# Performance work log

Measured on AMD Instinct MI355X. Metric: run time of the kernel, lower is better.

Reference implementation:

```python
import jax, jax.numpy as jnp
import numpy as np

_LOG2PI = float(np.log(2.0 * np.pi))


def setup_inputs() -> dict:
    key = jax.random.key(0)
    ks = jax.random.split(key, 9)
    B, T, S, A, O = 64, 128, 512, 16, 4096
    regime = jax.random.randint(ks[0], (B,), 0, 2).astype(jnp.float32)
    obs = jax.random.randint(ks[1], (T + 1, B), 0, O, dtype=jnp.int32)
    rewards = jax.random.normal(ks[2], (T + 1, B), jnp.float32)
    dones = jnp.zeros((T + 1, B), jnp.float32)
    actions = jax.random.randint(ks[3], (T, B), 0, A, dtype=jnp.int32)
    prior_logits = jax.random.normal(ks[4], (S,), jnp.float32)
    trans_logits = jax.random.normal(ks[5], (A, S, S), jnp.float32)
    obs_logits = jax.random.normal(ks[6], (S, O), jnp.float32)
    policy_logits = jax.random.normal(ks[7], (S, A), jnp.float32)
    r_mu = jax.random.normal(ks[8], (S,), jnp.float32)
    r_logsig = jnp.zeros((S,), jnp.float32)
    return {"regime": regime, "obs": obs, "rewards": rewards, "dones": dones,
            "actions": actions, "prior_logits": prior_logits,
            "trans_logits": trans_logits, "obs_logits": obs_logits,
            "policy_logits": policy_logits, "r_mu": r_mu, "r_logsig": r_logsig}


def _log_prob(regime, obs, rewards, dones, actions, prior_logits, trans_logits,
              obs_logits, policy_logits, r_mu, r_logsig):
    # normalized log-prob tables (tabular instantiation of AugmentedModel)
    log_prior = jax.nn.log_softmax(prior_logits)              # [S]
    log_trans = jax.nn.log_softmax(trans_logits, axis=-1)     # [A,S,S]
    log_obs = jax.nn.log_softmax(obs_logits, axis=-1)         # [S,O]
    log_pol = jax.nn.log_softmax(policy_logits, axis=-1)      # [S,A]
    lse = jax.scipy.special.logsumexp

    def emis(o, r):  # log q(o|s) + log q(r|s) -> [B,S]
        lo = log_obs.T[o]                                      # [B,S] gather
        lr = (-0.5 * (((r[:, None] - r_mu[None, :]) * jnp.exp(-r_logsig)[None, :]) ** 2)
              - r_logsig[None, :] - 0.5 * _LOG2PI)             # [B,S]
        return lo + lr

    def act_term(a, done):  # masked log q(a|s) -> [B,S]
        la = log_pol.T[a]                                      # [B,S]
        la = jnp.where((done == 1.0)[:, None], jnp.zeros_like(la), la)
        la = jnp.where((regime == 1.0)[:, None], jnp.zeros_like(la), la)
        return la

    T = actions.shape[0]
    B = regime.shape[0]

    # t = 0
    was_done = jnp.zeros((B,), rewards.dtype)
    done0 = dones[0]
    lq_sorda = log_prior[None, :] + emis(obs[0], rewards[0]) + act_term(actions[0], done0)
    lq_orda = lse(lq_sorda, axis=-1) * (1.0 - was_done)        # [B]
    log_prob = lq_orda
    lq_s_h = lq_sorda - lq_orda[:, None]
    # belief propagation through transition: [B,S,1] + [B,S,S] -> lse over prev state
    lq_snext_h = lse(lq_s_h[:, :, None] + log_trans[actions[0]], axis=1)

    def step(carry, xs):  # t = 1 .. T-1 (has an action)
        log_prob, was_done, lq_s_hprev = carry
        o, r, d, a = xs
        done = jnp.maximum(was_done, d)
        lq = lq_s_hprev + emis(o, r) + act_term(a, done)
        lq_orda = lse(lq, axis=-1) * (1.0 - was_done)
        log_prob = jnp.where(jnp.isinf(log_prob), log_prob, log_prob + lq_orda)
        lq_s_h = lq - lq_orda[:, None]
        lq_snext = lse(lq_s_h[:, :, None] + log_trans[a], axis=1)
        return (log_prob, done, lq_snext), None

    xs = (obs[1:T], rewards[1:T], dones[1:T], actions[1:T])
    (log_prob, was_done, lq_s_hprev), _ = jax.lax.scan(
        step, (log_prob, done0, lq_snext_h), xs)

    # final step t = T (no action term)
    lq = lq_s_hprev + emis(obs[T], rewards[T])
    lq_ord = lse(lq, axis=-1) * (1.0 - was_done)
    log_prob = jnp.where(jnp.isinf(log_prob), log_prob, log_prob + lq_ord)
    return log_prob


def reference(regime, obs, rewards, dones, actions, prior_logits, trans_logits,
              obs_logits, policy_logits, r_mu, r_logsig):
    return _log_prob(regime, obs, rewards, dones, actions, prior_logits,
                     trans_logits, obs_logits, policy_logits, r_mu, r_logsig)
```

## Files before the change

### kernel.cpp

```cpp
#include <hip/hip_runtime.h>
#include <math.h>

#define DI __device__ __forceinline__

constexpr int BB = 64;
constexpr int TT = 128;
constexpr int SS = 512;
constexpr int AA = 16;
constexpr int OO = 4096;
constexpr float LOG2PI = 1.8378770664093453f;
constexpr float LOG4096 = 8.317766166719343f;

typedef float f32x4 __attribute__((ext_vector_type(4)));

DI void lds_barrier() {
    asm volatile("s_waitcnt lgkmcnt(0)\n\ts_barrier" ::: "memory");
}

DI unsigned int f32_to_e4m3(float x) {
    unsigned int u = __float_as_uint(x);
    unsigned int lsb = (u >> 20) & 1u;
    unsigned int rounded = u + 0x7ffffu + lsb;
    int e8 = (int)(rounded >> 23) - 120;
    unsigned int m3 = (rounded >> 20) & 7u;
    unsigned int norm = ((unsigned int)e8 << 3) | m3;
    int sub = __float2int_rn(x * 512.0f);
    return (e8 <= 0) ? (unsigned int)sub : norm;
}

DI float bflyMax(float v) {
#pragma unroll
    for (int off = 32; off; off >>= 1) v = fmaxf(v, __shfl_xor(v, off));
    return v;
}
DI float bflySum(float v) {
#pragma unroll
    for (int off = 32; off; off >>= 1) v += __shfl_xor(v, off);
    return v;
}
DI float halfMax(float v) {
#pragma unroll
    for (int off = 16; off; off >>= 1) v = fmaxf(v, __shfl_xor(v, off));
    return v;
}
DI float halfSum(float v) {
#pragma unroll
    for (int off = 16; off; off >>= 1) v += __shfl_xor(v, off);
    return v;
}

template <int NW>
DI float blockMax(float v, float* wr) {
    v = bflyMax(v);
    const int lane = threadIdx.x & 63, wv = threadIdx.x >> 6;
    if (lane == 0) wr[wv] = v;
    __syncthreads();
    float r = wr[0];
#pragma unroll
    for (int i = 1; i < NW; ++i) r = fmaxf(r, wr[i]);
    __syncthreads();
    return r;
}
template <int NW>
DI float blockSum(float v, float* wr) {
    v = bflySum(v);
    const int lane = threadIdx.x & 63, wv = threadIdx.x >> 6;
    if (lane == 0) wr[wv] = v;
    __syncthreads();
    float r = wr[0];
#pragma unroll
    for (int i = 1; i < NW; ++i) r += wr[i];
    __syncthreads();
    return r;
}


__global__ __launch_bounds__(1024) void k_pack(const float* __restrict__ tl,
                                               unsigned char* __restrict__ PB) {
    __shared__ unsigned char lds[16384];
    const int a = blockIdx.x >> 4;
    const int kt = blockIdx.x & 15;
    const int tid = threadIdx.x;
    const int r = tid >> 5;
    const int nt = tid & 31;
    const int k = kt * 32 + r;
    const float* row = tl + ((size_t)a * SS + k) * SS + nt * 16;

    float x[16];
#pragma unroll
    for (int i = 0; i < 4; ++i) {
        float4 v = ((const float4*)row)[i];
        x[4 * i] = v.x; x[4 * i + 1] = v.y; x[4 * i + 2] = v.z; x[4 * i + 3] = v.w;
    }
    float mx = -INFINITY;
#pragma unroll
    for (int i = 0; i < 16; ++i) mx = fmaxf(mx, x[i]);
    mx = halfMax(mx);
    float e[16];
    float sm = 0.f;
#pragma unroll
    for (int i = 0; i < 16; ++i) { e[i] = __expf(x[i] - mx); sm += e[i]; }
    sm = halfSum(sm);
    const float scale = 256.0f / sm;

    const int base = (nt >> 1) * 1024 + ((r >> 3) * 16) * 16 + (nt & 1) * 8 + (r & 7);
#pragma unroll
    for (int i = 0; i < 16; ++i) {
        lds[base + i * 16] = (unsigned char)f32_to_e4m3(e[i] * scale);
    }
    __syncthreads();

    ulonglong2* dst = (ulonglong2*)(PB + (size_t)(a * 16 + kt) * 16384);
    dst[tid] = ((const ulonglong2*)lds)[tid];
}

__global__ __launch_bounds__(256) void k_obs_stats(const float* __restrict__ ol,
                                                   float* __restrict__ mo,
                                                   float* __restrict__ lo) {
    __shared__ float wr[4];
    const int s = blockIdx.x;
    const float* in = ol + (size_t)s * OO;
    const int tid = threadIdx.x;
    float mx = -INFINITY;
    for (int i = tid; i < OO; i += 256) mx = fmaxf(mx, in[i]);
    float m = blockMax<4>(mx, wr);
    float sm = 0.f;
    for (int i = tid; i < OO; i += 256) sm += __expf(in[i] - m);
    float sum = blockSum<4>(sm, wr);
    if (tid == 0) { mo[s] = m; lo[s] = __logf(sum); }
}

__global__ __launch_bounds__(256) void k_obsT(const float* __restrict__ ol,
                                              const float* __restrict__ mo,
                                              const float* __restrict__ lo,
                                              float* __restrict__ obsT) {
    __shared__ float tile[64][65];
    const int tO = blockIdx.x % (OO / 64);
    const int tS = blockIdx.x / (OO / 64);
    const int o0 = tO * 64, s0 = tS * 64;
    const int cc = threadIdx.x & 63, rr = threadIdx.x >> 6;
#pragma unroll
    for (int j = 0; j < 16; ++j) {
        int r = rr + j * 4;
        tile[r][cc] = ol[(size_t)(s0 + r) * OO + o0 + cc] - mo[s0 + r] - lo[s0 + r];
    }
    __syncthreads();
#pragma unroll
    for (int j = 0; j < 16; ++j) {
        int r = rr + j * 4;
        obsT[(size_t)(o0 + r) * SS + s0 + cc] = tile[cc][r];
    }
}

__global__ __launch_bounds__(512, 2) void k_main(
    const float* __restrict__ regime, const int* __restrict__ obs,
    const float* __restrict__ rewards, const float* __restrict__ dones,
    const int* __restrict__ actions, const float* __restrict__ prior_logits,
    const unsigned char* __restrict__ PB, const float* __restrict__ obsT,
    const float* __restrict__ policy_logits, const float* __restrict__ r_mu,
    const float* __restrict__ r_logsig, float* __restrict__ out) {
    __shared__ float wrm[8], wrs[8];
    __shared__ unsigned char p8[4 * 144 + 16];
    __shared__ float lqprev[SS];
    __shared__ float polT_l[AA * SS];
    __shared__ int obs_l[TT + 1];
    __shared__ float rew_l[TT + 1];
    __shared__ float done_l[TT + 1];
    __shared__ int act_l[TT];

    const int b = blockIdx.x;
    const int tid = threadIdx.x;
    const int wv = tid >> 6, lane = tid & 63, quad = lane >> 4;
    const int s = tid;

    if (tid <= TT) {
        obs_l[tid] = obs[tid * BB + b];
        rew_l[tid] = rewards[tid * BB + b];
        done_l[tid] = dones[tid * BB + b];
        if (tid < TT) act_l[tid] = actions[tid * BB + b];
    }
    {
        const float4* pr4 = (const float4*)(policy_logits + (size_t)s * AA);
        float4 v0 = pr4[0], v1 = pr4[1], v2 = pr4[2], v3 = pr4[3];
        float xv[16] = {v0.x, v0.y, v0.z, v0.w, v1.x, v1.y, v1.z, v1.w,
                        v2.x, v2.y, v2.z, v2.w, v3.x, v3.y, v3.z, v3.w};
        float mx = xv[0];
#pragma unroll
        for (int i = 1; i < 16; ++i) mx = fmaxf(mx, xv[i]);
        float sm = 0.f;
#pragma unroll
        for (int i = 0; i < 16; ++i) sm += __expf(xv[i] - mx);
        float ls = mx + __logf(sm);
#pragma unroll
        for (int a = 0; a < AA; ++a) polT_l[a * SS + s] = xv[a] - ls;
    }
    const float rm = r_mu[s];
    const float rls = r_logsig[s];
    const float inv_sig = __expf(-rls);
    const float reg = regime[b];

    float px = prior_logits[s];
    {
        float wm0 = bflyMax(px);
        if (lane == 0) wrm[wv] = wm0;
    }
    lds_barrier();
    float pm = wrm[0];
#pragma unroll
    for (int i = 1; i < 8; ++i) pm = fmaxf(pm, wrm[i]);
    {
        float ws0 = bflySum(__expf(px - pm));
        if (lane == 0) wrs[wv] = ws0;
    }
    lds_barrier();
    float psum = wrs[0];
#pragma unroll
    for (int i = 1; i < 8; ++i) psum += wrs[i];
    const float prior_reg = px - pm - __logf(psum);

    float obsv = obsT[(size_t)obs_l[0] * SS + s];

    float log_prob = 0.f;
    float was_done = 0.f;

    for (int t = 0; t < TT; ++t) {
        const float r = rew_l[t];
        const int a = act_l[t];
        const float d = done_l[t];
        const float done = fmaxf(was_done, d);

        const ulonglong2* PBa =
            (const ulonglong2*)(PB + (size_t)a * (SS * SS)) + 2 * wv * 64 + lane;
        ulonglong2 bfA[16], bfB[16];
#pragma unroll
        for (int kt = 0; kt < 16; ++kt) {
            bfA[kt] = PBa[kt * 16 * 64];
            bfB[kt] = PBa[kt * 16 * 64 + 64];
        }
        float obsv_next = obsT[(size_t)obs_l[t + 1] * SS + s];
        __builtin_amdgcn_sched_barrier(0);

        float diff = (r - rm) * inv_sig;
        float emis = obsv - 0.5f * diff * diff - rls - 0.5f * LOG2PI;
        float base_in = (t == 0) ? prior_reg : lqprev[s];
        float la = polT_l[a * SS + s];
        if (done == 1.0f || reg == 1.0f) la = 0.f;
        float lq = base_in + emis + la;

        float wmax = bflyMax(lq);
        if (lane == 0) wrm[wv] = wmax;
        lds_barrier();

        float m = wrm[0];
#pragma unroll
        for (int i = 1; i < 8; ++i) m = fmaxf(m, wrm[i]);

        float ex = __expf(lq - m);
        p8[((s >> 3) & 3) * 144 + (s >> 5) * 8 + (s & 7)] =
            (unsigned char)f32_to_e4m3(ex * 16.0f);
        float wsum = bflySum(ex);
        if (lane == 0) wrs[wv] = wsum;
        lds_barrier();

        float sum = wrs[0];
#pragma unroll
        for (int i = 1; i < 8; ++i) sum += wrs[i];
        float lse = m + __logf(sum);
        float lq_orda = lse * (1.0f - was_done);
        if (!isinf(log_prob)) log_prob += lq_orda;
        was_done = done;

        const float basev = m - lq_orda - LOG4096;
        f32x4 acc0 = {0.f, 0.f, 0.f, 0.f};
        f32x4 acc1 = {0.f, 0.f, 0.f, 0.f};
        f32x4 acc2 = {0.f, 0.f, 0.f, 0.f};
        f32x4 acc3 = {0.f, 0.f, 0.f, 0.f};
#pragma unroll
        for (int kt = 0; kt < 16; ++kt) {
            long af = *(const long long*)(p8 + quad * 144 + kt * 8);
            acc0 = __builtin_amdgcn_mfma_f32_16x16x32_fp8_fp8((long)bfA[kt].x, af, acc0, 0, 0, 0);
            acc1 = __builtin_amdgcn_mfma_f32_16x16x32_fp8_fp8((long)bfA[kt].y, af, acc1, 0, 0, 0);
            acc2 = __builtin_amdgcn_mfma_f32_16x16x32_fp8_fp8((long)bfB[kt].x, af, acc2, 0, 0, 0);
            acc3 = __builtin_amdgcn_mfma_f32_16x16x32_fp8_fp8((long)bfB[kt].y, af, acc3, 0, 0, 0);
        }
        if (lane < 16) {
            lqprev[wv * 64 + lane]      = basev + __logf(acc0[0]);
            lqprev[wv * 64 + 16 + lane] = basev + __logf(acc1[0]);
            lqprev[wv * 64 + 32 + lane] = basev + __logf(acc2[0]);
            lqprev[wv * 64 + 48 + lane] = basev + __logf(acc3[0]);
        }
        lds_barrier();
        obsv = obsv_next;
    }

    {
        const float r = rew_l[TT];
        float diff = (r - rm) * inv_sig;
        float emis = obsv - 0.5f * diff * diff - rls - 0.5f * LOG2PI;
        float lq = lqprev[s] + emis;
        float wmax = bflyMax(lq);
        if (lane == 0) wrm[wv] = wmax;
        lds_barrier();
        float m = wrm[0];
#pragma unroll
        for (int i = 1; i < 8; ++i) m = fmaxf(m, wrm[i]);
        float wsum = bflySum(__expf(lq - m));
        if (lane == 0) wrs[wv] = wsum;
        lds_barrier();
        float sum = wrs[0];
#pragma unroll
        for (int i = 1; i < 8; ++i) sum += wrs[i];
        float lse = m + __logf(sum);
        float lq_ord = lse * (1.0f - was_done);
        if (!isinf(log_prob)) log_prob += lq_ord;
    }

    if (tid == 0) out[b] = log_prob;
}

extern "C" void kernel_launch(void* const* d_in, const int* in_sizes, int n_in,
                              void* d_out, int out_size, void* d_ws, size_t ws_size,
                              hipStream_t stream) {
    const float* regime = (const float*)d_in[0];
    const int* obs = (const int*)d_in[1];
    const float* rewards = (const float*)d_in[2];
    const float* dones = (const float*)d_in[3];
    const int* actions = (const int*)d_in[4];
    const float* prior_logits = (const float*)d_in[5];
    const float* trans_logits = (const float*)d_in[6];
    const float* obs_logits = (const float*)d_in[7];
    const float* policy_logits = (const float*)d_in[8];
    const float* r_mu = (const float*)d_in[9];
    const float* r_logsig = (const float*)d_in[10];
    float* out = (float*)d_out;

    char* ws = (char*)d_ws;
    unsigned char* PB = (unsigned char*)ws;
    float* obsT = (float*)(ws + (size_t)AA * SS * SS);
    float* mo = (float*)(ws + (size_t)AA * SS * SS + (size_t)OO * SS * 4);
    float* lo = mo + SS;

    k_pack<<<256, 1024, 0, stream>>>(trans_logits, PB);
    k_obs_stats<<<SS, 256, 0, stream>>>(obs_logits, mo, lo);
    k_obsT<<<(OO / 64) * (SS / 64), 256, 0, stream>>>(obs_logits, mo, lo, obsT);
    k_main<<<BB, 512, 0, stream>>>(regime, obs, rewards, dones, actions, prior_logits,
                                   PB, obsT, policy_logits, r_mu, r_logsig, out);
}
```

Measured before the change: 568.6 us.

## Split each batch row across four cooperating blocks with global-memory step barrier

Each batch element is now handled by four workgroups, and each one computes a quarter of the next-state columns of the per-step transition matmul. Partial results go to a double-buffered global exchange array, and an atomic counter acts as a per-batch barrier before every step. The trans matrix is repacked so each wave reads a contiguous 128 KB slice per action. This cuts per-block MFMA and load work by four and uses 256 blocks instead of 64. In exchange it adds a global atomic spin-wait every timestep, and it relies on all four blocks being co-resident, which risks deadlock if they are not.

```diff
diff --git a/kernel.cpp b/kernel.cpp
--- a/kernel.cpp
+++ b/kernel.cpp
@@ -110,8 +110,15 @@
     }
     __syncthreads();
 
-    ulonglong2* dst = (ulonglong2*)(PB + (size_t)(a * 16 + kt) * 16384);
-    dst[tid] = ((const ulonglong2*)lds)[tid];
+#pragma unroll
+    for (int c = 0; c < 2; ++c) {
+        int idx = tid + c * 1024;
+        int n = idx >> 6, lane = idx & 63;
+        unsigned long long v =
+            *(const unsigned long long*)(lds + (n >> 1) * 1024 + lane * 16 + (n & 1) * 8);
+        *(unsigned long long*)(PB + (size_t)a * 262144 + n * 8192 +
+                               (kt >> 1) * 1024 + lane * 16 + (kt & 1) * 8) = v;
+    }
 }
 
 __global__ __launch_bounds__(256) void k_obs_stats(const float* __restrict__ ol,
@@ -152,26 +159,31 @@
     }
 }
 
+__global__ void k_init(unsigned int* cnt) { cnt[threadIdx.x] = 0u; }
+
 __global__ __launch_bounds__(512, 2) void k_main(
     const float* __restrict__ regime, const int* __restrict__ obs,
     const float* __restrict__ rewards, const float* __restrict__ dones,
     const int* __restrict__ actions, const float* __restrict__ prior_logits,
     const unsigned char* __restrict__ PB, const float* __restrict__ obsT,
     const float* __restrict__ policy_logits, const float* __restrict__ r_mu,
-    const float* __restrict__ r_logsig, float* __restrict__ out) {
+    const float* __restrict__ r_logsig, float* ex, unsigned int* cnt,
+    float* __restrict__ out) {
     __shared__ float wrm[8], wrs[8];
     __shared__ unsigned char p8[4 * 144 + 16];
-    __shared__ float lqprev[SS];
     __shared__ float polT_l[AA * SS];
     __shared__ int obs_l[TT + 1];
     __shared__ float rew_l[TT + 1];
     __shared__ float done_l[TT + 1];
     __shared__ int act_l[TT];
 
-    const int b = blockIdx.x;
+    const int gb = blockIdx.x;
+    const int b = gb >> 2;
+    const int j = gb & 3;
     const int tid = threadIdx.x;
     const int wv = tid >> 6, lane = tid & 63, quad = lane >> 4;
     const int s = tid;
+    const int n = j * 8 + wv;
 
     if (tid <= TT) {
         obs_l[tid] = obs[tid * BB + b];
@@ -220,29 +232,27 @@
 
     float obsv = obsT[(size_t)obs_l[0] * SS + s];
 
+    float lq_reg = 0.f;
     float log_prob = 0.f;
     float was_done = 0.f;
 
     for (int t = 0; t < TT; ++t) {
         const float r = rew_l[t];
-        const int a = act_l[t];
+        const int a = __builtin_amdgcn_readfirstlane(act_l[t]);
         const float d = done_l[t];
         const float done = fmaxf(was_done, d);
 
-        const ulonglong2* PBa =
-            (const ulonglong2*)(PB + (size_t)a * (SS * SS)) + 2 * wv * 64 + lane;
-        ulonglong2 bfA[16], bfB[16];
-#pragma unroll
-        for (int kt = 0; kt < 16; ++kt) {
-            bfA[kt] = PBa[kt * 16 * 64];
-            bfB[kt] = PBa[kt * 16 * 64 + 64];
-        }
+        const unsigned char* base = PB + (size_t)a * 262144 + n * 8192 + lane * 16;
+        ulonglong2 bf[8];
+#pragma unroll
+        for (int ktp = 0; ktp < 8; ++ktp)
+            bf[ktp] = *(const ulonglong2*)(base + ktp * 1024);
         float obsv_next = obsT[(size_t)obs_l[t + 1] * SS + s];
         __builtin_amdgcn_sched_barrier(0);
 
         float diff = (r - rm) * inv_sig;
         float emis = obsv - 0.5f * diff * diff - rls - 0.5f * LOG2PI;
-        float base_in = (t == 0) ? prior_reg : lqprev[s];
+        float base_in = (t == 0) ? prior_reg : lq_reg;
         float la = polT_l[a * SS + s];
         if (done == 1.0f || reg == 1.0f) la = 0.f;
         float lq = base_in + emis + la;
@@ -250,18 +260,16 @@
         float wmax = bflyMax(lq);
         if (lane == 0) wrm[wv] = wmax;
         lds_barrier();
-
         float m = wrm[0];
 #pragma unroll
         for (int i = 1; i < 8; ++i) m = fmaxf(m, wrm[i]);
 
-        float ex = __expf(lq - m);
+        float exv = __expf(lq - m);
         p8[((s >> 3) & 3) * 144 + (s >> 5) * 8 + (s & 7)] =
-            (unsigned char)f32_to_e4m3(ex * 16.0f);
-        float wsum = bflySum(ex);
+            (unsigned char)f32_to_e4m3(exv * 16.0f);
+        float wsum = bflySum(exv);
         if (lane == 0) wrs[wv] = wsum;
         lds_barrier();
-
         float sum = wrs[0];
 #pragma unroll
         for (int i = 1; i < 8; ++i) sum += wrs[i];
@@ -271,25 +279,31 @@
         was_done = done;
 
         const float basev = m - lq_orda - LOG4096;
-        f32x4 acc0 = {0.f, 0.f, 0.f, 0.f};
-        f32x4 acc1 = {0.f, 0.f, 0.f, 0.f};
-        f32x4 acc2 = {0.f, 0.f, 0.f, 0.f};
-        f32x4 acc3 = {0.f, 0.f, 0.f, 0.f};
+        f32x4 acc = {0.f, 0.f, 0.f, 0.f};
 #pragma unroll
         for (int kt = 0; kt < 16; ++kt) {
             long af = *(const long long*)(p8 + quad * 144 + kt * 8);
-            acc0 = __builtin_amdgcn_mfma_f32_16x16x32_fp8_fp8((long)bfA[kt].x, af, acc0, 0, 0, 0);
-            acc1 = __builtin_amdgcn_mfma_f32_16x16x32_fp8_fp8((long)bfA[kt].y, af, acc1, 0, 0, 0);
-            acc2 = __builtin_amdgcn_mfma_f32_16x16x32_fp8_fp8((long)bfB[kt].x, af, acc2, 0, 0, 0);
-            acc3 = __builtin_amdgcn_mfma_f32_16x16x32_fp8_fp8((long)bfB[kt].y, af, acc3, 0, 0, 0);
+            long bh = (kt & 1) ? (long)bf[kt >> 1].y : (long)bf[kt >> 1].x;
+            acc = __builtin_amdgcn_mfma_f32_16x16x32_fp8_fp8(bh, af, acc, 0, 0, 0);
         }
+        float* exb = ex + ((size_t)(t & 1) * BB + b) * SS;
         if (lane < 16) {
-            lqprev[wv * 64 + lane]      = basev + __logf(acc0[0]);
-            lqprev[wv * 64 + 16 + lane] = basev + __logf(acc1[0]);
-            lqprev[wv * 64 + 32 + lane] = basev + __logf(acc2[0]);
-            lqprev[wv * 64 + 48 + lane] = basev + __logf(acc3[0]);
+            __hip_atomic_store(&exb[n * 16 + lane], basev + __logf(acc[0]),
+                               __ATOMIC_RELAXED, __HIP_MEMORY_SCOPE_AGENT);
         }
-        lds_barrier();
+        __syncthreads();
+
+        if (tid == 0) {
+            __hip_atomic_fetch_add(&cnt[b], 1u, __ATOMIC_RELEASE,
+                                   __HIP_MEMORY_SCOPE_AGENT);
+            const unsigned target = 4u * (unsigned)(t + 1);
+            while (__hip_atomic_load(&cnt[b], __ATOMIC_ACQUIRE,
+                                     __HIP_MEMORY_SCOPE_AGENT) < target)
+                __builtin_amdgcn_s_sleep(1);
+        }
+        lds_barrier();
+        lq_reg = __hip_atomic_load(&exb[s], __ATOMIC_RELAXED,
+                                   __HIP_MEMORY_SCOPE_AGENT);
         obsv = obsv_next;
     }
 
@@ -297,7 +311,7 @@
         const float r = rew_l[TT];
         float diff = (r - rm) * inv_sig;
         float emis = obsv - 0.5f * diff * diff - rls - 0.5f * LOG2PI;
-        float lq = lqprev[s] + emis;
+        float lq = lq_reg + emis;
         float wmax = bflyMax(lq);
         if (lane == 0) wrm[wv] = wmax;
         lds_barrier();
@@ -315,7 +329,7 @@
         if (!isinf(log_prob)) log_prob += lq_ord;
     }
 
-    if (tid == 0) out[b] = log_prob;
+    if (j == 0 && tid == 0) out[b] = log_prob;
 }
 
 extern "C" void kernel_launch(void* const* d_in, const int* in_sizes, int n_in,
@@ -339,10 +353,14 @@
     float* obsT = (float*)(ws + (size_t)AA * SS * SS);
     float* mo = (float*)(ws + (size_t)AA * SS * SS + (size_t)OO * SS * 4);
     float* lo = mo + SS;
-
+    unsigned int* cnt = (unsigned int*)(lo + SS);
+    float* ex = (float*)(cnt + 64);
+
+    k_init<<<1, 64, 0, stream>>>(cnt);
     k_pack<<<256, 1024, 0, stream>>>(trans_logits, PB);
     k_obs_stats<<<SS, 256, 0, stream>>>(obs_logits, mo, lo);
     k_obsT<<<(OO / 64) * (SS / 64), 256, 0, stream>>>(obs_logits, mo, lo, obsT);
-    k_main<<<BB, 512, 0, stream>>>(regime, obs, rewards, dones, actions, prior_logits,
-                                   PB, obsT, policy_logits, r_mu, r_logsig, out);
-}
+    k_main<<<BB * 4, 512, 0, stream>>>(regime, obs, rewards, dones, actions,
+                                       prior_logits, PB, obsT, policy_logits,
+                                       r_mu, r_logsig, ex, cnt, out);
+}
```

After: 1.652 ms. 191% more time.

## Stream transition tiles through LDS with async global_load_lds triple buffering

Applied to the files above, without the earlier changes.

Replaces the per-step register prefetch of all sixteen fp8 transition B-fragments with a three-deep ring of direct global-to-LDS loads (global_load_lds) per wave, issuing the next chunk as each chunk's MFMAs run. The policy log-softmax table moves out of shared memory into sixteen registers per thread, with the action picked by a select chain, and launch bounds drop the two-blocks-per-CU hint. The aim is to cut register pressure from the 32 ulonglong2 prefetch buffers and overlap the transition fetch with the MFMA chain. In exchange it uses 48KB more LDS and adds hand-placed vmcnt and lgkmcnt waits, and the vmcnt counts look fragile given the extra obsT load issued after the first DMAs.

```diff
diff --git a/kernel.cpp b/kernel.cpp
--- a/kernel.cpp
+++ b/kernel.cpp
@@ -15,6 +15,12 @@
 
 DI void lds_barrier() {
     asm volatile("s_waitcnt lgkmcnt(0)\n\ts_barrier" ::: "memory");
+}
+
+typedef __attribute__((address_space(3))) unsigned int as3_u32;
+typedef __attribute__((address_space(1))) const unsigned int as1_u32;
+DI void dma1k(const unsigned char* g, unsigned char* l) {
+    __builtin_amdgcn_global_load_lds((as1_u32*)g, (as3_u32*)l, 16, 0, 0);
 }
 
 DI unsigned int f32_to_e4m3(float x) {
@@ -152,17 +158,17 @@
     }
 }
 
-__global__ __launch_bounds__(512, 2) void k_main(
+__global__ __launch_bounds__(512) void k_main(
     const float* __restrict__ regime, const int* __restrict__ obs,
     const float* __restrict__ rewards, const float* __restrict__ dones,
     const int* __restrict__ actions, const float* __restrict__ prior_logits,
     const unsigned char* __restrict__ PB, const float* __restrict__ obsT,
     const float* __restrict__ policy_logits, const float* __restrict__ r_mu,
     const float* __restrict__ r_logsig, float* __restrict__ out) {
+    __shared__ unsigned char stage[3 * 16384];
     __shared__ float wrm[8], wrs[8];
     __shared__ unsigned char p8[4 * 144 + 16];
     __shared__ float lqprev[SS];
-    __shared__ float polT_l[AA * SS];
     __shared__ int obs_l[TT + 1];
     __shared__ float rew_l[TT + 1];
     __shared__ float done_l[TT + 1];
@@ -179,20 +185,23 @@
         done_l[tid] = dones[tid * BB + b];
         if (tid < TT) act_l[tid] = actions[tid * BB + b];
     }
+    float la16[16];
     {
         const float4* pr4 = (const float4*)(policy_logits + (size_t)s * AA);
         float4 v0 = pr4[0], v1 = pr4[1], v2 = pr4[2], v3 = pr4[3];
-        float xv[16] = {v0.x, v0.y, v0.z, v0.w, v1.x, v1.y, v1.z, v1.w,
-                        v2.x, v2.y, v2.z, v2.w, v3.x, v3.y, v3.z, v3.w};
-        float mx = xv[0];
-#pragma unroll
-        for (int i = 1; i < 16; ++i) mx = fmaxf(mx, xv[i]);
+        la16[0] = v0.x; la16[1] = v0.y; la16[2] = v0.z; la16[3] = v0.w;
+        la16[4] = v1.x; la16[5] = v1.y; la16[6] = v1.z; la16[7] = v1.w;
+        la16[8] = v2.x; la16[9] = v2.y; la16[10] = v2.z; la16[11] = v2.w;
+        la16[12] = v3.x; la16[13] = v3.y; la16[14] = v3.z; la16[15] = v3.w;
+        float mx = la16[0];
+#pragma unroll
+        for (int i = 1; i < 16; ++i) mx = fmaxf(mx, la16[i]);
         float sm = 0.f;
 #pragma unroll
-        for (int i = 0; i < 16; ++i) sm += __expf(xv[i] - mx);
+        for (int i = 0; i < 16; ++i) sm += __expf(la16[i] - mx);
         float ls = mx + __logf(sm);
 #pragma unroll
-        for (int a = 0; a < AA; ++a) polT_l[a * SS + s] = xv[a] - ls;
+        for (int i = 0; i < 16; ++i) la16[i] -= ls;
     }
     const float rm = r_mu[s];
     const float rls = r_logsig[s];
@@ -225,43 +234,46 @@
 
     for (int t = 0; t < TT; ++t) {
         const float r = rew_l[t];
-        const int a = act_l[t];
+        const int a = __builtin_amdgcn_readfirstlane(act_l[t]);
         const float d = done_l[t];
         const float done = fmaxf(was_done, d);
 
-        const ulonglong2* PBa =
-            (const ulonglong2*)(PB + (size_t)a * (SS * SS)) + 2 * wv * 64 + lane;
-        ulonglong2 bfA[16], bfB[16];
-#pragma unroll
-        for (int kt = 0; kt < 16; ++kt) {
-            bfA[kt] = PBa[kt * 16 * 64];
-            bfB[kt] = PBa[kt * 16 * 64 + 64];
+        const unsigned char* PBa = PB + (size_t)a * (16 * 16384);
+        unsigned char* mystage = stage + wv * 2048;
+
+#pragma unroll
+        for (int c = 0; c < 3; ++c) {
+            const unsigned char* g = PBa + c * 16384 + (2 * wv) * 1024 + lane * 16;
+            unsigned char* l = mystage + c * 16384;
+            dma1k(g, l);
+            dma1k(g + 1024, l + 1024);
         }
+        asm volatile("" ::: "memory");
         float obsv_next = obsT[(size_t)obs_l[t + 1] * SS + s];
-        __builtin_amdgcn_sched_barrier(0);
+        asm volatile("" ::: "memory");
 
         float diff = (r - rm) * inv_sig;
         float emis = obsv - 0.5f * diff * diff - rls - 0.5f * LOG2PI;
         float base_in = (t == 0) ? prior_reg : lqprev[s];
-        float la = polT_l[a * SS + s];
+        float la = la16[0];
+#pragma unroll
+        for (int i = 1; i < 16; ++i) la = (a == i) ? la16[i] : la;
         if (done == 1.0f || reg == 1.0f) la = 0.f;
         float lq = base_in + emis + la;
 
         float wmax = bflyMax(lq);
         if (lane == 0) wrm[wv] = wmax;
         lds_barrier();
-
         float m = wrm[0];
 #pragma unroll
         for (int i = 1; i < 8; ++i) m = fmaxf(m, wrm[i]);
 
-        float ex = __expf(lq - m);
+        float exv = __expf(lq - m);
         p8[((s >> 3) & 3) * 144 + (s >> 5) * 8 + (s & 7)] =
-            (unsigned char)f32_to_e4m3(ex * 16.0f);
-        float wsum = bflySum(ex);
+            (unsigned char)f32_to_e4m3(exv * 16.0f);
+        float wsum = bflySum(exv);
         if (lane == 0) wrs[wv] = wsum;
         lds_barrier();
-
         float sum = wrs[0];
 #pragma unroll
         for (int i = 1; i < 8; ++i) sum += wrs[i];
@@ -275,14 +287,32 @@
         f32x4 acc1 = {0.f, 0.f, 0.f, 0.f};
         f32x4 acc2 = {0.f, 0.f, 0.f, 0.f};
         f32x4 acc3 = {0.f, 0.f, 0.f, 0.f};
-#pragma unroll
-        for (int kt = 0; kt < 16; ++kt) {
-            long af = *(const long long*)(p8 + quad * 144 + kt * 8);
-            acc0 = __builtin_amdgcn_mfma_f32_16x16x32_fp8_fp8((long)bfA[kt].x, af, acc0, 0, 0, 0);
-            acc1 = __builtin_amdgcn_mfma_f32_16x16x32_fp8_fp8((long)bfA[kt].y, af, acc1, 0, 0, 0);
-            acc2 = __builtin_amdgcn_mfma_f32_16x16x32_fp8_fp8((long)bfB[kt].x, af, acc2, 0, 0, 0);
-            acc3 = __builtin_amdgcn_mfma_f32_16x16x32_fp8_fp8((long)bfB[kt].y, af, acc3, 0, 0, 0);
+
+#define CHUNK(c, WN)                                                            \
+        {                                                                       \
+            asm volatile("s_waitcnt vmcnt(" #WN ")" ::: "memory");              \
+            const unsigned char* sb = mystage + ((c) % 3) * 16384 + lane * 16;  \
+            ulonglong2 f0 = *(const ulonglong2*)(sb);                           \
+            ulonglong2 f1 = *(const ulonglong2*)(sb + 1024);                    \
+            long af = *(const long long*)(p8 + quad * 144 + (c) * 8);           \
+            acc0 = __builtin_amdgcn_mfma_f32_16x16x32_fp8_fp8((long)f0.x, af, acc0, 0, 0, 0); \
+            acc1 = __builtin_amdgcn_mfma_f32_16x16x32_fp8_fp8((long)f0.y, af, acc1, 0, 0, 0); \
+            acc2 = __builtin_amdgcn_mfma_f32_16x16x32_fp8_fp8((long)f1.x, af, acc2, 0, 0, 0); \
+            acc3 = __builtin_amdgcn_mfma_f32_16x16x32_fp8_fp8((long)f1.y, af, acc3, 0, 0, 0); \
+            if ((c) + 3 < 16) {                                                 \
+                asm volatile("s_waitcnt lgkmcnt(0)" ::: "memory");              \
+                const unsigned char* g = PBa + ((c) + 3) * 16384 + (2 * wv) * 1024 + lane * 16; \
+                unsigned char* l = mystage + ((c) % 3) * 16384;                 \
+                dma1k(g, l);                                                    \
+                dma1k(g + 1024, l + 1024);                                      \
+            }                                                                   \
         }
+        CHUNK(0, 5)  CHUNK(1, 5)  CHUNK(2, 5)  CHUNK(3, 4)
+        CHUNK(4, 4)  CHUNK(5, 4)  CHUNK(6, 4)  CHUNK(7, 4)
+        CHUNK(8, 4)  CHUNK(9, 4)  CHUNK(10, 4) CHUNK(11, 4)
+        CHUNK(12, 4) CHUNK(13, 4) CHUNK(14, 2) CHUNK(15, 0)
+#undef CHUNK
+
         if (lane < 16) {
             lqprev[wv * 64 + lane]      = basev + __logf(acc0[0]);
             lqprev[wv * 64 + 16 + lane] = basev + __logf(acc1[0]);
```

Result: faster. 539.2 us (-5.2%).
